# Optimization experiments

Hardware: AMD Instinct MI355X
Metric: run time of the kernel (lower is better)

## Reference

```python
import jax, jax.numpy as jnp
import numpy as np

N = 100000   # nodes
E = 800000   # undirected (unique) edges; directed count = 2*E
DV = 128; DE = 16; DH = 128; DO = 128
G = 64       # graphs in batch


def setup_inputs() -> dict:
    key = jax.random.key(0)
    ks = jax.random.split(key, 8)
    x = jax.random.normal(ks[0], (N, DV), jnp.float32)
    edge_index = jax.random.randint(ks[1], (2, 2 * E), 0, N, dtype=jnp.int32)
    edge_attr = jax.random.normal(ks[2], (E, DE), jnp.float32)
    batch = jnp.sort(jax.random.randint(ks[3], (N,), 0, G, dtype=jnp.int32))
    s = lambda k, shp, fan: jax.random.normal(k, shp, jnp.float32) / np.sqrt(fan)
    W_gcn = s(ks[4], (DV, DH), DV); b_gcn = jnp.zeros((DH,), jnp.float32)
    W_le = s(ks[5], (DE, DH), DE); b_le = jnp.zeros((DH,), jnp.float32)
    W_lin = s(ks[6], (2 * DH, DH), 2 * DH); b_lin = jnp.zeros((DH,), jnp.float32)
    W_out = s(ks[7], (DH, DO), DH); b_out = jnp.zeros((DO,), jnp.float32)
    return dict(x=x, edge_index=edge_index, edge_attr=edge_attr, batch=batch,
                W_gcn=W_gcn, b_gcn=b_gcn, W_le=W_le, b_le=b_le,
                W_lin=W_lin, b_lin=b_lin, W_out=W_out, b_out=b_out)


def reference(x, edge_index, edge_attr, batch,
              W_gcn, b_gcn, W_le, b_le, W_lin, b_lin, W_out, b_out):
    n = x.shape[0]
    loop = jnp.arange(n, dtype=edge_index.dtype)
    src = jnp.concatenate([edge_index[0], loop])  # [2E+N] with self loops
    dst = jnp.concatenate([edge_index[1], loop])

    # ---- GCNConv: symmetric norm, self-loops, lin then aggregate, + bias ----
    xw = x @ W_gcn                                      # [N, DH]
    ones_e = jnp.ones(src.shape[0], jnp.float32)
    deg = jax.ops.segment_sum(ones_e, dst, num_segments=n)  # >=1 via self loops
    dinv = jax.lax.rsqrt(deg)
    norm = dinv[src] * dinv[dst]                        # [2E+N]
    h = jax.ops.segment_sum(norm[:, None] * xw[src], dst, num_segments=n) + b_gcn
    h = jax.nn.relu(h)

    # ---- EdgeGCN: duplicate edge_attr per direction, self-loop attr = ones ----
    ea2 = jnp.repeat(edge_attr, 2, axis=0)              # [2E, DE] interleaved
    ea_full = jnp.concatenate([ea2, jnp.ones((n, edge_attr.shape[1]), jnp.float32)])
    edge_feat = ea_full @ W_le + b_le                   # [2E+N, DH]
    x_j = h[src]                                        # gather source node feats
    msg = jnp.concatenate([x_j, edge_feat], axis=-1) @ W_lin + b_lin
    h2 = jax.ops.segment_sum(msg, dst, num_segments=n)  # aggr='add'
    h2 = jax.nn.relu(h2)

    # ---- global mean pool + final linear ----
    cnt = jax.ops.segment_sum(jnp.ones(n, jnp.float32), batch, num_segments=G)
    pooled = jax.ops.segment_sum(h2, batch, num_segments=G) / jnp.maximum(cnt, 1.0)[:, None]
    return pooled @ W_out + b_out                       # [G, DO]
```

## Files before the change

### kernel.cpp

```cpp
#include <hip/hip_runtime.h>
#include <hip/hip_bf16.h>
#include <cstddef>

typedef unsigned int  u32;
typedef unsigned short u16;
typedef __attribute__((ext_vector_type(8))) short short8;
typedef __attribute__((ext_vector_type(4))) float f32x4;
typedef __attribute__((ext_vector_type(2))) float f32x2;

#define DV 128
#define DH 128
#define DE 16
#define DO 128

__device__ inline float bf_lo(u32 u){ return __uint_as_float(u << 16); }
__device__ inline float bf_hi(u32 u){ return __uint_as_float(u & 0xFFFF0000u); }
__device__ inline u32 fpack2(float a, float b){
  u32 ua = __float_as_uint(a), ub = __float_as_uint(b);
  ua += 0x7FFFu + ((ua >> 16) & 1u);
  ub += 0x7FFFu + ((ub >> 16) & 1u);
  return (ua >> 16) | (ub & 0xFFFF0000u);
}
__device__ inline u16 f2bf(float a){
  u32 ua = __float_as_uint(a); ua += 0x7FFFu + ((ua >> 16) & 1u); return (u16)(ua >> 16);
}

__device__ inline void acc_fp8v(u32 s, f32x2& lo, f32x2& hi){
  lo += __builtin_amdgcn_cvt_pk_f32_fp8((int)s, false);
  hi += __builtin_amdgcn_cvt_pk_f32_fp8((int)s, true);
}
__device__ inline u32 pack_fp8(float a0, float a1, float a2, float a3){
  int o = __builtin_amdgcn_cvt_pk_fp8_f32(a0, a1, 0, false);
  o = __builtin_amdgcn_cvt_pk_fp8_f32(a2, a3, o, true);
  return (u32)o;
}

__global__ void k_init(int* cnt, float* poolp, u32* xws_zrow, u32* h_zrow, int n, int pn){
  int v = blockIdx.x * blockDim.x + threadIdx.x;
  if (v < n) cnt[v] = 0;
  if (v < pn) poolp[v] = 0.f;
  if (v < 32){ xws_zrow[v] = 0u; h_zrow[v] = 0u; }
}

__global__ void k_count(const int* dst, const float* edge_attr, int* cnt, int* rank,
                        u32* ea_pack, int2* ce, int e2, int cefill, int nmark){
  int j = blockIdx.x * blockDim.x + threadIdx.x;
  int tot = gridDim.x * blockDim.x;
  if (j < e2){
    rank[j] = atomicAdd(&cnt[dst[j]], 1);
    float4 f0 = *(const float4*)(edge_attr + (size_t)j * 8);
    float4 f1 = *(const float4*)(edge_attr + (size_t)j * 8 + 4);
    uint4 o;
    o.x = fpack2(f0.x, f0.y); o.y = fpack2(f0.z, f0.w);
    o.z = fpack2(f1.x, f1.y); o.w = fpack2(f1.z, f1.w);
    *(uint4*)(ea_pack + (size_t)j * 4) = o;
  }
  int2 pd = make_int2(nmark, 0);
  for (int i = j; i < cefill; i += tot) ce[i] = pd;
}

__global__ __launch_bounds__(256) void k_scan1(const int* cnt, int* partial, int* bsums, int n){
  __shared__ int lds[256];
  int t = threadIdx.x;
  int base = blockIdx.x * 1024 + t * 4;
  int v0=0,v1=0,v2=0,v3=0;
  if (base + 3 < n){ int4 q = *(const int4*)(cnt + base); v0=q.x; v1=q.y; v2=q.z; v3=q.w; }
  else {
    if (base + 0 < n) v0 = cnt[base];
    if (base + 1 < n) v1 = cnt[base+1];
    if (base + 2 < n) v2 = cnt[base+2];
  }
  v0 = (v0 + 7) & ~7; v1 = (v1 + 7) & ~7; v2 = (v2 + 7) & ~7; v3 = (v3 + 7) & ~7;
  v1 += v0; v2 += v1; v3 += v2;
  lds[t] = v3; __syncthreads();
  for (int off = 1; off < 256; off <<= 1){
    int x = (t >= off) ? lds[t - off] : 0;
    __syncthreads();
    lds[t] += x;
    __syncthreads();
  }
  int add = (t > 0) ? lds[t - 1] : 0;
  if (base + 3 < n){
    int4 q; q.x = v0+add; q.y = v1+add; q.z = v2+add; q.w = v3+add;
    *(int4*)(partial + base) = q;
  } else {
    if (base + 0 < n) partial[base]   = v0 + add;
    if (base + 1 < n) partial[base+1] = v1 + add;
    if (base + 2 < n) partial[base+2] = v2 + add;
  }
  if (t == 255) bsums[blockIdx.x] = lds[255];
}

__global__ __launch_bounds__(256) void k_scan3w(const int* partial, const int* bsums, int nb,
                                                int* row_ptr, const int* cnt,
                                                float* dinv, float* degf,
                                                const int* batch, int* startg, int n, int g, int NB,
                                                const float* W_lin, const float* b_lin,
                                                const float* W_le, const float* b_le, float* Wfull){
  int bid = blockIdx.x;
  int t = threadIdx.x;
  if (bid >= NB){
    int r = (bid - NB) * 2 + (t >> 7), c = t & 127;
    if (r < DH){
      Wfull[r * DH + c] = W_lin[r * DH + c];
    } else if (r < DH + DE){
      int i = r - DH;
      float acc = 0.f;
      #pragma unroll 8
      for (int k = 0; k < DH; k += 4){
        float4 wl = *(const float4*)(W_le + i * DH + k);
        acc += wl.x * W_lin[(size_t)(DH + k    ) * DH + c];
        acc += wl.y * W_lin[(size_t)(DH + k + 1) * DH + c];
        acc += wl.z * W_lin[(size_t)(DH + k + 2) * DH + c];
        acc += wl.w * W_lin[(size_t)(DH + k + 3) * DH + c];
      }
      Wfull[r * DH + c] = acc;
    } else if (r == 144){
      float acc = b_lin[c];
      #pragma unroll 8
      for (int k = 0; k < DH; k += 4){
        float4 bl = *(const float4*)(b_le + k);
        acc += bl.x * W_lin[(size_t)(DH + k    ) * DH + c];
        acc += bl.y * W_lin[(size_t)(DH + k + 1) * DH + c];
        acc += bl.z * W_lin[(size_t)(DH + k + 2) * DH + c];
        acc += bl.w * W_lin[(size_t)(DH + k + 3) * DH + c];
      }
      Wfull[r * DH + c] = acc;
    } else if (r < 160){
      Wfull[r * DH + c] = 0.f;
    }
    return;
  }
  __shared__ int lds[128];
  if (t < 128) lds[t] = (t < nb) ? bsums[t] : 0;
  __syncthreads();
  for (int off = 1; off < 128; off <<= 1){
    int x = (t >= off && t < 128) ? lds[t - off] : 0;
    __syncthreads();
    if (t < 128) lds[t] += x;
    __syncthreads();
  }
  int i = bid * 256 + t;
  if (i < n){
    int chunk = i >> 10;
    int add = (chunk > 0) ? lds[chunk - 1] : 0;
    row_ptr[i + 1] = partial[i] + add;
    if (i == 0) row_ptr[0] = 0;
    float c = (float)(cnt[i] + 1);
    dinv[i] = rsqrtf(c);
    degf[i] = c;
    int b = batch[i];
    int prev = (i == 0) ? -1 : batch[i - 1];
    for (int q = prev + 1; q <= b; ++q) startg[q] = i;
    if (i == n - 1){ for (int q = b + 1; q <= g; ++q) startg[q] = n; }
  }
}

__global__ __launch_bounds__(256) void k_scatter_g1(const int* src, const int* dst, const int* rank,
                                                    const int* row_ptr, int2* ce, int e2, int SB,
                                                    const float* x, const float* W,
                                                    const float* dinv, u32* xws8, int M){
  __shared__ u16 lds_u[64 * 136];
  int bid = blockIdx.x;
  int tid = threadIdx.x;
  if (bid < SB){
    int j = bid * 256 + tid;
    if (j < e2){
      int d = dst[j];
      int pos = row_ptr[d] + rank[j];
      ce[pos] = make_int2(src[j] << 5, j >> 1);
    }
    return;
  }
  int row0 = (bid - SB) * 64;
  u16* Wt = lds_u;
  u16* At = lds_u + 128 * 40;
  int l = tid & 63, w = tid >> 6;
  int m = l & 15, quad = l >> 4;
  f32x4 acc[8];
  #pragma unroll
  for (int ct = 0; ct < 8; ++ct) acc[ct] = (f32x4){0.f, 0.f, 0.f, 0.f};
  for (int ks = 0; ks < DV; ks += 32){
    __syncthreads();
    {
      int c = tid & 127, hh = tid >> 7;
      #pragma unroll
      for (int g2 = 0; g2 < 2; ++g2){
        int k0 = hh * 16 + g2 * 8;
        const float* Wp = W + (size_t)(ks + k0) * 128 + c;
        float w0 = Wp[0*128], w1 = Wp[1*128], w2 = Wp[2*128], w3 = Wp[3*128];
        float w4 = Wp[4*128], w5 = Wp[5*128], w6 = Wp[6*128], w7 = Wp[7*128];
        uint4 pk;
        pk.x = fpack2(w0, w1); pk.y = fpack2(w2, w3);
        pk.z = fpack2(w4, w5); pk.w = fpack2(w6, w7);
        *(uint4*)&Wt[c * 40 + k0] = pk;
      }
    }
    {
      int r = tid >> 2, ch = tid & 3;
      int gr = row0 + r; if (gr > M - 1) gr = M - 1;
      const float* A = x + (size_t)gr * DV + ks + ch * 8;
      float4 q0 = *(const float4*)A;
      float4 q1 = *(const float4*)(A + 4);
      uint4 pk;
      pk.x = fpack2(q0.x, q0.y); pk.y = fpack2(q0.z, q0.w);
      pk.z = fpack2(q1.x, q1.y); pk.w = fpack2(q1.z, q1.w);
      *(uint4*)&At[r * 40 + ch * 8] = pk;
    }
    __syncthreads();
    short8 av = *(const short8*)&At[(w * 16 + m) * 40 + quad * 8];
    #pragma unroll
    for (int ct = 0; ct < 8; ++ct){
      short8 bv = *(const short8*)&Wt[(ct * 16 + m) * 40 + quad * 8];
      acc[ct] = __builtin_amdgcn_mfma_f32_16x16x32_bf16(av, bv, acc[ct], 0, 0, 0);
    }
  }
  __syncthreads();
  u16* Ct = lds_u;
  float sc[4];
  #pragma unroll
  for (int r = 0; r < 4; ++r){
    int gr = row0 + w * 16 + quad * 4 + r;
    sc[r] = dinv[gr < M ? gr : (M - 1)];
  }
  #pragma unroll
  for (int ct = 0; ct < 8; ++ct){
    #pragma unroll
    for (int r = 0; r < 4; ++r){
      float vv = acc[ct][r] * sc[r];
      Ct[(w * 16 + quad * 4 + r) * 136 + ct * 16 + m] = f2bf(vv);
    }
  }
  __syncthreads();
  for (int idx = tid; idx < 64 * 16; idx += 256){
    int r = idx >> 4, c8 = idx & 15;
    int gr = row0 + r;
    if (gr < M){
      uint4 qv = *(const uint4*)&Ct[r * 136 + c8 * 8];
      uint2 ov;
      ov.x = (u32)__builtin_amdgcn_cvt_pk_fp8_f32(bf_lo(qv.y), bf_hi(qv.y),
             __builtin_amdgcn_cvt_pk_fp8_f32(bf_lo(qv.x), bf_hi(qv.x), 0, false), true);
      ov.y = (u32)__builtin_amdgcn_cvt_pk_fp8_f32(bf_lo(qv.w), bf_hi(qv.w),
             __builtin_amdgcn_cvt_pk_fp8_f32(bf_lo(qv.z), bf_hi(qv.z), 0, false), true);
      *(uint2*)(xws8 + (size_t)gr * 32 + c8 * 2) = ov;
    }
  }
}

__global__ __launch_bounds__(256) void k_gemm2_pool(const u16* A2b, const float* W, int M,
                                                    const int* batchp, float* poolp){
  __shared__ u16 lds_u[128 * 40 + 64 * 40];
  u16* Wt = lds_u;
  u16* At = lds_u + 128 * 40;
  int tid = threadIdx.x;
  int row0 = blockIdx.x * 64;
  int l = tid & 63, w = tid >> 6;
  int m = l & 15, quad = l >> 4;
  f32x4 acc[8];
  #pragma unroll
  for (int ct = 0; ct < 8; ++ct) acc[ct] = (f32x4){0.f, 0.f, 0.f, 0.f};
  for (int ks = 0; ks < 160; ks += 32){
    __syncthreads();
    {
      int c = tid & 127, hh = tid >> 7;
      #pragma unroll
      for (int g2 = 0; g2 < 2; ++g2){
        int k0 = hh * 16 + g2 * 8;
        const float* Wp = W + (size_t)(ks + k0) * 128 + c;
        float w0 = Wp[0*128], w1 = Wp[1*128], w2 = Wp[2*128], w3 = Wp[3*128];
        float w4 = Wp[4*128], w5 = Wp[5*128], w6 = Wp[6*128], w7 = Wp[7*128];
        uint4 pk;
        pk.x = fpack2(w0, w1); pk.y = fpack2(w2, w3);
        pk.z = fpack2(w4, w5); pk.w = fpack2(w6, w7);
        *(uint4*)&Wt[c * 40 + k0] = pk;
      }
    }
    {
      int r = tid >> 2, ch = tid & 3;
      int gr = row0 + r; if (gr > M - 1) gr = M - 1;
      uint4 pk = *(const uint4*)(A2b + (size_t)gr * 160 + ks + ch * 8);
      *(uint4*)&At[r * 40 + ch * 8] = pk;
    }
    __syncthreads();
    short8 av = *(const short8*)&At[(w * 16 + m) * 40 + quad * 8];
    #pragma unroll
    for (int ct = 0; ct < 8; ++ct){
      short8 bv = *(const short8*)&Wt[(ct * 16 + m) * 40 + quad * 8];
      acc[ct] = __builtin_amdgcn_mfma_f32_16x16x32_bf16(av, bv, acc[ct], 0, 0, 0);
    }
  }
  __syncthreads();

  float* ps = (float*)lds_u;
  int rbase = w * 16 + quad * 4;
  int g0 = batchp[row0];
  int glast = batchp[(row0 + 63 < M) ? (row0 + 63) : (M - 1)];
  if (g0 == glast){
    #pragma unroll
    for (int ct = 0; ct < 8; ++ct){
      float s = 0.f;
      #pragma unroll
      for (int r = 0; r < 4; ++r){
        float vv = fmaxf(acc[ct][r], 0.f);
        if (row0 + rbase + r < M) s += vv;
      }
      s += __shfl_xor(s, 16);
      s += __shfl_xor(s, 32);
      if (quad == 0) ps[w * 128 + ct * 16 + m] = s;
    }
    __syncthreads();
    if (tid < 128){
      float t = ps[tid] + ps[128 + tid] + ps[256 + tid] + ps[384 + tid];
      atomicAdd(&poolp[g0 * DO + tid], t);
    }
  } else {
    #pragma unroll
    for (int ct = 0; ct < 8; ++ct){
      #pragma unroll
      for (int r = 0; r < 4; ++r){
        int row = row0 + rbase + r;
        if (row < M){
          float vv = fmaxf(acc[ct][r], 0.f);
          atomicAdd(&poolp[batchp[row] * DO + ct * 16 + m], vv);
        }
      }
    }
  }
}

__global__ __launch_bounds__(256) void k_phase1(const u32* xws8, const int* row_ptr, const int2* ce,
                                                const float* dinv, const float* b_gcn, u32* h8, int n){
  int lane = threadIdx.x & 63;
  int ln = lane & 31;
  int v = blockIdx.x * 8 + ((threadIdx.x >> 6) << 1) + (lane >> 5);
  if (v >= n) return;
  u32 sp = xws8[(size_t)v * 32 + ln];
  f32x2 aLo = (f32x2){0.f, 0.f}, aHi = (f32x2){0.f, 0.f};
  acc_fp8v(sp, aLo, aHi);
  int e0 = row_ptr[v], e1 = row_ptr[v + 1];
  int B = (e1 - e0) >> 3;
  const int4* cp = (const int4*)(ce + e0);
  u32 q0=0,q1=0,q2=0,q3=0,q4=0,q5=0,q6=0,q7=0;
  u32 r0=0,r1=0,r2=0,r3=0,r4=0,r5=0,r6=0,r7=0;
  if (B > 0){
    int4 A = cp[0], Bb = cp[1], C = cp[2], D = cp[3];
    q0 = xws8[A.x + ln]; q1 = xws8[A.z + ln];
    q2 = xws8[Bb.x + ln]; q3 = xws8[Bb.z + ln];
    q4 = xws8[C.x + ln]; q5 = xws8[C.z + ln];
    q6 = xws8[D.x + ln]; q7 = xws8[D.z + ln];
  }
  if (B > 1){
    int4 A = cp[4], Bb = cp[5], C = cp[6], D = cp[7];
    r0 = xws8[A.x + ln]; r1 = xws8[A.z + ln];
    r2 = xws8[Bb.x + ln]; r3 = xws8[Bb.z + ln];
    r4 = xws8[C.x + ln]; r5 = xws8[C.z + ln];
    r6 = xws8[D.x + ln]; r7 = xws8[D.z + ln];
  }
  for (int k = 0; k + 2 < B; ++k){
    const int4* cpp = cp + (size_t)(k + 2) * 4;
    int4 A = cpp[0], Bb = cpp[1], C = cpp[2], D = cpp[3];
    u32 p0 = xws8[A.x + ln], p1 = xws8[A.z + ln];
    u32 p2 = xws8[Bb.x + ln], p3 = xws8[Bb.z + ln];
    u32 p4 = xws8[C.x + ln], p5 = xws8[C.z + ln];
    u32 p6 = xws8[D.x + ln], p7 = xws8[D.z + ln];
    acc_fp8v(q0, aLo, aHi); acc_fp8v(q1, aLo, aHi);
    acc_fp8v(q2, aLo, aHi); acc_fp8v(q3, aLo, aHi);
    acc_fp8v(q4, aLo, aHi); acc_fp8v(q5, aLo, aHi);
    acc_fp8v(q6, aLo, aHi); acc_fp8v(q7, aLo, aHi);
    q0=r0; q1=r1; q2=r2; q3=r3; q4=r4; q5=r5; q6=r6; q7=r7;
    r0=p0; r1=p1; r2=p2; r3=p3; r4=p4; r5=p5; r6=p6; r7=p7;
  }
  if (B > 1){
    acc_fp8v(q0, aLo, aHi); acc_fp8v(q1, aLo, aHi);
    acc_fp8v(q2, aLo, aHi); acc_fp8v(q3, aLo, aHi);
    acc_fp8v(q4, aLo, aHi); acc_fp8v(q5, aLo, aHi);
    acc_fp8v(q6, aLo, aHi); acc_fp8v(q7, aLo, aHi);
    q0=r0; q1=r1; q2=r2; q3=r3; q4=r4; q5=r5; q6=r6; q7=r7;
  }
  if (B > 0){
    acc_fp8v(q0, aLo, aHi); acc_fp8v(q1, aLo, aHi);
    acc_fp8v(q2, aLo, aHi); acc_fp8v(q3, aLo, aHi);
    acc_fp8v(q4, aLo, aHi); acc_fp8v(q5, aLo, aHi);
    acc_fp8v(q6, aLo, aHi); acc_fp8v(q7, aLo, aHi);
  }
  float dv = dinv[v];
  float4 bg = *(const float4*)(b_gcn + ln * 4);
  float a0 = fmaxf(fmaf(dv, aLo.x, bg.x), 0.f);
  float a1 = fmaxf(fmaf(dv, aLo.y, bg.y), 0.f);
  float a2 = fmaxf(fmaf(dv, aHi.x, bg.z), 0.f);
  float a3 = fmaxf(fmaf(dv, aHi.y, bg.w), 0.f);
  h8[(size_t)v * 32 + ln] = pack_fp8(a0, a1, a2, a3);
}

__global__ __launch_bounds__(256) void k_phase2(const u32* h8, const int* row_ptr, const int2* ce,
                                                const u16* ea_bf, const float* degf,
                                                u16* A2b, int n){
  int lane = threadIdx.x & 63;
  int ln = lane & 31;
  int half = lane >> 5;
  int v = blockIdx.x * 8 + ((threadIdx.x >> 6) << 1) + half;
  if (v >= n) return;
  u32 sp = h8[(size_t)v * 32 + ln];
  f32x2 aLo = (f32x2){0.f, 0.f}, aHi = (f32x2){0.f, 0.f};
  acc_fp8v(sp, aLo, aHi);
  float es = 0.f;
  int ch = ln & 15, grp = ln >> 4;
  int nmark = n << 5;
  int e0 = row_ptr[v], e1 = row_ptr[v + 1];
  int i = e0;
  u32 q0=0,q1=0,q2=0,q3=0,q4=0,q5=0,q6=0,q7=0;
  float w0=0.f,w1=0.f,w2=0.f,w3=0.f;
  float m0=0.f,m1=0.f,m2=0.f,m3=0.f;
  if (i < e1){
    const int4* cp = (const int4*)(ce + i);
    int4 A = cp[0], B = cp[1], C = cp[2], D = cp[3];
    q0 = h8[A.x + ln]; q1 = h8[A.z + ln];
    q2 = h8[B.x + ln]; q3 = h8[B.z + ln];
    q4 = h8[C.x + ln]; q5 = h8[C.z + ln];
    q6 = h8[D.x + ln]; q7 = h8[D.z + ln];
    int s0x = grp ? C.x : A.x, s0e = grp ? C.y : A.y;
    int s1x = grp ? C.z : A.z, s1e = grp ? C.w : A.w;
    int s2x = grp ? D.x : B.x, s2e = grp ? D.y : B.y;
    int s3x = grp ? D.z : B.z, s3e = grp ? D.w : B.w;
    w0 = bf_lo((u32)ea_bf[(size_t)s0e * 16 + ch]);
    w1 = bf_lo((u32)ea_bf[(size_t)s1e * 16 + ch]);
    w2 = bf_lo((u32)ea_bf[(size_t)s2e * 16 + ch]);
    w3 = bf_lo((u32)ea_bf[(size_t)s3e * 16 + ch]);
    m0 = (s0x != nmark) ? 1.f : 0.f;
    m1 = (s1x != nmark) ? 1.f : 0.f;
    m2 = (s2x != nmark) ? 1.f : 0.f;
    m3 = (s3x != nmark) ? 1.f : 0.f;
  }
  for (; i + 8 < e1; i += 8){
    const int4* cp2 = (const int4*)(ce + i + 8);
    int4 A2 = cp2[0], B2 = cp2[1], C2 = cp2[2], D2 = cp2[3];
    int t0x = grp ? C2.x : A2.x, t0e = grp ? C2.y : A2.y;
    int t1x = grp ? C2.z : A2.z, t1e = grp ? C2.w : A2.w;
    int t2x = grp ? D2.x : B2.x, t2e = grp ? D2.y : B2.y;
    int t3x = grp ? D2.z : B2.z, t3e = grp ? D2.w : B2.w;
    float u0 = bf_lo((u32)ea_bf[(size_t)t0e * 16 + ch]);
    float u1 = bf_lo((u32)ea_bf[(size_t)t1e * 16 + ch]);
    float u2 = bf_lo((u32)ea_bf[(size_t)t2e * 16 + ch]);
    float u3 = bf_lo((u32)ea_bf[(size_t)t3e * 16 + ch]);
    float n0 = (t0x != nmark) ? 1.f : 0.f;
    float n1 = (t1x != nmark) ? 1.f : 0.f;
    float n2 = (t2x != nmark) ? 1.f : 0.f;
    float n3 = (t3x != nmark) ? 1.f : 0.f;
    u32 p0 = h8[A2.x + ln], p1 = h8[A2.z + ln];
    u32 p2 = h8[B2.x + ln], p3 = h8[B2.z + ln];
    u32 p4 = h8[C2.x + ln], p5 = h8[C2.z + ln];
    u32 p6 = h8[D2.x + ln], p7 = h8[D2.z + ln];
    acc_fp8v(q0, aLo, aHi); acc_fp8v(q1, aLo, aHi);
    acc_fp8v(q2, aLo, aHi); acc_fp8v(q3, aLo, aHi);
    acc_fp8v(q4, aLo, aHi); acc_fp8v(q5, aLo, aHi);
    acc_fp8v(q6, aLo, aHi); acc_fp8v(q7, aLo, aHi);
    es = fmaf(m0, w0, es);
    es = fmaf(m1, w1, es);
    es = fmaf(m2, w2, es);
    es = fmaf(m3, w3, es);
    q0=p0; q1=p1; q2=p2; q3=p3; q4=p4; q5=p5; q6=p6; q7=p7;
    w0=u0; w1=u1; w2=u2; w3=u3;
    m0=n0; m1=n1; m2=n2; m3=n3;
  }
  if (i < e1){
    acc_fp8v(q0, aLo, aHi); acc_fp8v(q1, aLo, aHi);
    acc_fp8v(q2, aLo, aHi); acc_fp8v(q3, aLo, aHi);
    acc_fp8v(q4, aLo, aHi); acc_fp8v(q5, aLo, aHi);
    acc_fp8v(q6, aLo, aHi); acc_fp8v(q7, aLo, aHi);
    es = fmaf(m0, w0, es);
    es = fmaf(m1, w1, es);
    es = fmaf(m2, w2, es);
    es = fmaf(m3, w3, es);
  }
  es += __shfl_xor(es, 16);
  float c0v = __shfl(es, half * 32 + (ln & 7) * 2);
  float c1v = __shfl(es, half * 32 + (ln & 7) * 2 + 1);
  u32* rowp = (u32*)(A2b + (size_t)v * 160);
  uint2 o; o.x = fpack2(aLo.x, aLo.y); o.y = fpack2(aHi.x, aHi.y);
  *(uint2*)(rowp + ln * 2) = o;
  if (ln < 8){
    rowp[64 + ln] = fpack2(c0v + 1.0f, c1v + 1.0f);
  } else if (ln < 16){
    rowp[64 + ln] = (ln == 8) ? (u32)f2bf(degf[v]) : 0u;
  }
}

__global__ __launch_bounds__(128) void k_poolb_final(const float* poolp, const int* start,
                                                     const float* W_out, const float* b_out,
                                                     float* out){
  __shared__ float pl[DH];
  int g = blockIdx.x, c = threadIdx.x;
  int cntg = start[g + 1] - start[g]; if (cntg < 1) cntg = 1;
  pl[c] = poolp[g * DO + c] / (float)cntg;
  __syncthreads();
  float acc = b_out[c];
  for (int k = 0; k < DH; ++k) acc += pl[k] * W_out[k * DO + c];
  out[g * DO + c] = acc;
}

extern "C" void kernel_launch(void* const* d_in, const int* in_sizes, int n_in,
                              void* d_out, int out_size, void* d_ws, size_t ws_size,
                              hipStream_t stream){
  const float* x         = (const float*)d_in[0];
  const int*   edge_index= (const int*)  d_in[1];
  const float* edge_attr = (const float*)d_in[2];
  const int*   batch     = (const int*)  d_in[3];
  const float* W_gcn     = (const float*)d_in[4];
  const float* b_gcn     = (const float*)d_in[5];
  const float* W_le      = (const float*)d_in[6];
  const float* b_le      = (const float*)d_in[7];
  const float* W_lin     = (const float*)d_in[8];
  const float* b_lin     = (const float*)d_in[9];
  const float* W_out     = (const float*)d_in[10];
  const float* b_out     = (const float*)d_in[11];
  float* out = (float*)d_out;

  const int n  = in_sizes[0] / DV;
  const int e2 = in_sizes[1] / 2;
  const int g  = out_size / DO;
  const int* srcp = edge_index;
  const int* dstp = edge_index + e2;
  const int e2pad = e2 + 7 * n + 8;

  char* ws = (char*)d_ws;
  size_t off = 0;
  auto alloc = [&](size_t bytes) -> char* {
    char* p = ws + off; off = (off + bytes + 255) & ~(size_t)255; return p;
  };

  int*   cnt     = (int*)  alloc((size_t)n * 4);
  int*   row_ptr = (int*)  alloc((size_t)(n + 1) * 4);
  int*   rank    = (int*)  alloc((size_t)e2 * 4);
  int*   partial = (int*)  alloc((size_t)n * 4);
  int*   bsums   = (int*)  alloc(512);
  float* dinv    = (float*)alloc((size_t)n * 4);
  float* degf    = (float*)alloc((size_t)n * 4);
  int*   startg  = (int*)  alloc((size_t)(g + 1) * 4);
  float* poolp   = (float*)alloc((size_t)g * DO * 4);
  float* Wfull   = (float*)alloc(160 * DH * 4);
  u32*   h8      = (u32*)  alloc((size_t)(n + 1) * 128);
  int2*  ce      = (int2*) alloc((size_t)e2pad * 8);
  u32*   ea_bf   = (u32*)  alloc((size_t)e2 * 16);
  size_t szXW = (size_t)(n + 1) * 128, szA2 = (size_t)n * 160 * 2;
  char* regionA = alloc(szA2 > szXW ? szA2 : szXW);
  u32* xws8 = (u32*)regionA;
  u16* A2b  = (u16*)regionA;

  const int nb1024 = (n + 1023) / 1024;
  const int NB = (n + 255) / 256;
  const int SB = (e2 + 255) / 256;
  const int GB = (n + 63) / 64;

  k_init      <<<(n + 255) / 256, 256, 0, stream>>>(cnt, poolp,
                                                    xws8 + (size_t)n * 32, h8 + (size_t)n * 32,
                                                    n, g * DO);
  k_count     <<<SB, 256, 0, stream>>>(dstp, edge_attr, cnt, rank, ea_bf, ce,
                                       e2, e2pad, n << 5);
  k_scan1     <<<nb1024, 256, 0, stream>>>(cnt, partial, bsums, n);
  k_scan3w    <<<NB + 80, 256, 0, stream>>>(partial, bsums, nb1024, row_ptr, cnt, dinv, degf,
                                            batch, startg, n, g, NB,
                                            W_lin, b_lin, W_le, b_le, Wfull);
  k_scatter_g1<<<SB + GB, 256, 0, stream>>>(srcp, dstp, rank, row_ptr, ce, e2, SB,
                                            x, W_gcn, dinv, xws8, n);
  k_phase1    <<<(n + 7) / 8, 256, 0, stream>>>(xws8, row_ptr, ce, dinv, b_gcn, h8, n);
  k_phase2    <<<(n + 7) / 8, 256, 0, stream>>>(h8, row_ptr, ce,
                                                (const u16*)ea_bf, degf, A2b, n);
  k_gemm2_pool<<<GB, 256, 0, stream>>>(A2b, Wfull, n, batch, poolp);
  k_poolb_final<<<g, 128, 0, stream>>>(poolp, startg, W_out, b_out, out);
}
```

Before: 398.8 us.

## Fuse phase-2 edge aggregation with final GEMM and pooling via LDS staging

```diff
diff --git a/kernel.cpp b/kernel.cpp
--- a/kernel.cpp
+++ b/kernel.cpp
@@ -247,87 +247,6 @@
   }
 }
 
-__global__ __launch_bounds__(256) void k_gemm2_pool(const u16* A2b, const float* W, int M,
-                                                    const int* batchp, float* poolp){
-  __shared__ u16 lds_u[128 * 40 + 64 * 40];
-  u16* Wt = lds_u;
-  u16* At = lds_u + 128 * 40;
-  int tid = threadIdx.x;
-  int row0 = blockIdx.x * 64;
-  int l = tid & 63, w = tid >> 6;
-  int m = l & 15, quad = l >> 4;
-  f32x4 acc[8];
-  #pragma unroll
-  for (int ct = 0; ct < 8; ++ct) acc[ct] = (f32x4){0.f, 0.f, 0.f, 0.f};
-  for (int ks = 0; ks < 160; ks += 32){
-    __syncthreads();
-    {
-      int c = tid & 127, hh = tid >> 7;
-      #pragma unroll
-      for (int g2 = 0; g2 < 2; ++g2){
-        int k0 = hh * 16 + g2 * 8;
-        const float* Wp = W + (size_t)(ks + k0) * 128 + c;
-        float w0 = Wp[0*128], w1 = Wp[1*128], w2 = Wp[2*128], w3 = Wp[3*128];
-        float w4 = Wp[4*128], w5 = Wp[5*128], w6 = Wp[6*128], w7 = Wp[7*128];
-        uint4 pk;
-        pk.x = fpack2(w0, w1); pk.y = fpack2(w2, w3);
-        pk.z = fpack2(w4, w5); pk.w = fpack2(w6, w7);
-        *(uint4*)&Wt[c * 40 + k0] = pk;
-      }
-    }
-    {
-      int r = tid >> 2, ch = tid & 3;
-      int gr = row0 + r; if (gr > M - 1) gr = M - 1;
-      uint4 pk = *(const uint4*)(A2b + (size_t)gr * 160 + ks + ch * 8);
-      *(uint4*)&At[r * 40 + ch * 8] = pk;
-    }
-    __syncthreads();
-    short8 av = *(const short8*)&At[(w * 16 + m) * 40 + quad * 8];
-    #pragma unroll
-    for (int ct = 0; ct < 8; ++ct){
-      short8 bv = *(const short8*)&Wt[(ct * 16 + m) * 40 + quad * 8];
-      acc[ct] = __builtin_amdgcn_mfma_f32_16x16x32_bf16(av, bv, acc[ct], 0, 0, 0);
-    }
-  }
-  __syncthreads();
-
-  float* ps = (float*)lds_u;
-  int rbase = w * 16 + quad * 4;
-  int g0 = batchp[row0];
-  int glast = batchp[(row0 + 63 < M) ? (row0 + 63) : (M - 1)];
-  if (g0 == glast){
-    #pragma unroll
-    for (int ct = 0; ct < 8; ++ct){
-      float s = 0.f;
-      #pragma unroll
-      for (int r = 0; r < 4; ++r){
-        float vv = fmaxf(acc[ct][r], 0.f);
-        if (row0 + rbase + r < M) s += vv;
-      }
-      s += __shfl_xor(s, 16);
-      s += __shfl_xor(s, 32);
-      if (quad == 0) ps[w * 128 + ct * 16 + m] = s;
-    }
-    __syncthreads();
-    if (tid < 128){
-      float t = ps[tid] + ps[128 + tid] + ps[256 + tid] + ps[384 + tid];
-      atomicAdd(&poolp[g0 * DO + tid], t);
-    }
-  } else {
-    #pragma unroll
-    for (int ct = 0; ct < 8; ++ct){
-      #pragma unroll
-      for (int r = 0; r < 4; ++r){
-        int row = row0 + rbase + r;
-        if (row < M){
-          float vv = fmaxf(acc[ct][r], 0.f);
-          atomicAdd(&poolp[batchp[row] * DO + ct * 16 + m], vv);
-        }
-      }
-    }
-  }
-}
-
 __global__ __launch_bounds__(256) void k_phase1(const u32* xws8, const int* row_ptr, const int2* ce,
                                                 const float* dinv, const float* b_gcn, u32* h8, int n){
   int lane = threadIdx.x & 63;
@@ -392,96 +311,177 @@
   h8[(size_t)v * 32 + ln] = pack_fp8(a0, a1, a2, a3);
 }
 
-__global__ __launch_bounds__(256) void k_phase2(const u32* h8, const int* row_ptr, const int2* ce,
+__global__ __launch_bounds__(256) void k_p2gemm(const u32* h8, const int* row_ptr, const int2* ce,
                                                 const u16* ea_bf, const float* degf,
-                                                u16* A2b, int n){
-  int lane = threadIdx.x & 63;
+                                                const float* W, int n,
+                                                const int* batchp, float* poolp){
+  __shared__ u16 At2[64 * 172];
+  __shared__ u16 Wt[128 * 40];
+  int tid = threadIdx.x;
+  int lane = tid & 63;
   int ln = lane & 31;
   int half = lane >> 5;
-  int v = blockIdx.x * 8 + ((threadIdx.x >> 6) << 1) + half;
-  if (v >= n) return;
-  u32 sp = h8[(size_t)v * 32 + ln];
-  f32x2 aLo = (f32x2){0.f, 0.f}, aHi = (f32x2){0.f, 0.f};
-  acc_fp8v(sp, aLo, aHi);
-  float es = 0.f;
+  int row0 = blockIdx.x * 64;
   int ch = ln & 15, grp = ln >> 4;
   int nmark = n << 5;
-  int e0 = row_ptr[v], e1 = row_ptr[v + 1];
-  int i = e0;
-  u32 q0=0,q1=0,q2=0,q3=0,q4=0,q5=0,q6=0,q7=0;
-  float w0=0.f,w1=0.f,w2=0.f,w3=0.f;
-  float m0=0.f,m1=0.f,m2=0.f,m3=0.f;
-  if (i < e1){
-    const int4* cp = (const int4*)(ce + i);
-    int4 A = cp[0], B = cp[1], C = cp[2], D = cp[3];
-    q0 = h8[A.x + ln]; q1 = h8[A.z + ln];
-    q2 = h8[B.x + ln]; q3 = h8[B.z + ln];
-    q4 = h8[C.x + ln]; q5 = h8[C.z + ln];
-    q6 = h8[D.x + ln]; q7 = h8[D.z + ln];
-    int s0x = grp ? C.x : A.x, s0e = grp ? C.y : A.y;
-    int s1x = grp ? C.z : A.z, s1e = grp ? C.w : A.w;
-    int s2x = grp ? D.x : B.x, s2e = grp ? D.y : B.y;
-    int s3x = grp ? D.z : B.z, s3e = grp ? D.w : B.w;
-    w0 = bf_lo((u32)ea_bf[(size_t)s0e * 16 + ch]);
-    w1 = bf_lo((u32)ea_bf[(size_t)s1e * 16 + ch]);
-    w2 = bf_lo((u32)ea_bf[(size_t)s2e * 16 + ch]);
-    w3 = bf_lo((u32)ea_bf[(size_t)s3e * 16 + ch]);
-    m0 = (s0x != nmark) ? 1.f : 0.f;
-    m1 = (s1x != nmark) ? 1.f : 0.f;
-    m2 = (s2x != nmark) ? 1.f : 0.f;
-    m3 = (s3x != nmark) ? 1.f : 0.f;
-  }
-  for (; i + 8 < e1; i += 8){
-    const int4* cp2 = (const int4*)(ce + i + 8);
-    int4 A2 = cp2[0], B2 = cp2[1], C2 = cp2[2], D2 = cp2[3];
-    int t0x = grp ? C2.x : A2.x, t0e = grp ? C2.y : A2.y;
-    int t1x = grp ? C2.z : A2.z, t1e = grp ? C2.w : A2.w;
-    int t2x = grp ? D2.x : B2.x, t2e = grp ? D2.y : B2.y;
-    int t3x = grp ? D2.z : B2.z, t3e = grp ? D2.w : B2.w;
-    float u0 = bf_lo((u32)ea_bf[(size_t)t0e * 16 + ch]);
-    float u1 = bf_lo((u32)ea_bf[(size_t)t1e * 16 + ch]);
-    float u2 = bf_lo((u32)ea_bf[(size_t)t2e * 16 + ch]);
-    float u3 = bf_lo((u32)ea_bf[(size_t)t3e * 16 + ch]);
-    float n0 = (t0x != nmark) ? 1.f : 0.f;
-    float n1 = (t1x != nmark) ? 1.f : 0.f;
-    float n2 = (t2x != nmark) ? 1.f : 0.f;
-    float n3 = (t3x != nmark) ? 1.f : 0.f;
-    u32 p0 = h8[A2.x + ln], p1 = h8[A2.z + ln];
-    u32 p2 = h8[B2.x + ln], p3 = h8[B2.z + ln];
-    u32 p4 = h8[C2.x + ln], p5 = h8[C2.z + ln];
-    u32 p6 = h8[D2.x + ln], p7 = h8[D2.z + ln];
-    acc_fp8v(q0, aLo, aHi); acc_fp8v(q1, aLo, aHi);
-    acc_fp8v(q2, aLo, aHi); acc_fp8v(q3, aLo, aHi);
-    acc_fp8v(q4, aLo, aHi); acc_fp8v(q5, aLo, aHi);
-    acc_fp8v(q6, aLo, aHi); acc_fp8v(q7, aLo, aHi);
-    es = fmaf(m0, w0, es);
-    es = fmaf(m1, w1, es);
-    es = fmaf(m2, w2, es);
-    es = fmaf(m3, w3, es);
-    q0=p0; q1=p1; q2=p2; q3=p3; q4=p4; q5=p5; q6=p6; q7=p7;
-    w0=u0; w1=u1; w2=u2; w3=u3;
-    m0=n0; m1=n1; m2=n2; m3=n3;
-  }
-  if (i < e1){
-    acc_fp8v(q0, aLo, aHi); acc_fp8v(q1, aLo, aHi);
-    acc_fp8v(q2, aLo, aHi); acc_fp8v(q3, aLo, aHi);
-    acc_fp8v(q4, aLo, aHi); acc_fp8v(q5, aLo, aHi);
-    acc_fp8v(q6, aLo, aHi); acc_fp8v(q7, aLo, aHi);
-    es = fmaf(m0, w0, es);
-    es = fmaf(m1, w1, es);
-    es = fmaf(m2, w2, es);
-    es = fmaf(m3, w3, es);
-  }
-  es += __shfl_xor(es, 16);
-  float c0v = __shfl(es, half * 32 + (ln & 7) * 2);
-  float c1v = __shfl(es, half * 32 + (ln & 7) * 2 + 1);
-  u32* rowp = (u32*)(A2b + (size_t)v * 160);
-  uint2 o; o.x = fpack2(aLo.x, aLo.y); o.y = fpack2(aHi.x, aHi.y);
-  *(uint2*)(rowp + ln * 2) = o;
-  if (ln < 8){
-    rowp[64 + ln] = fpack2(c0v + 1.0f, c1v + 1.0f);
-  } else if (ln < 16){
-    rowp[64 + ln] = (ln == 8) ? (u32)f2bf(degf[v]) : 0u;
+
+  for (int pass = 0; pass < 8; ++pass){
+    int local = pass * 8 + ((tid >> 6) << 1) + half;
+    int v = row0 + local;
+    u32* rowp = (u32*)&At2[(size_t)local * 172];
+    if (v >= n){
+      rowp[ln] = 0u; rowp[ln + 32] = 0u;
+      if (ln < 22) rowp[ln + 64] = 0u;
+      continue;
+    }
+    u32 sp = h8[(size_t)v * 32 + ln];
+    f32x2 aLo = (f32x2){0.f, 0.f}, aHi = (f32x2){0.f, 0.f};
+    acc_fp8v(sp, aLo, aHi);
+    float es = 0.f;
+    int e0 = row_ptr[v], e1 = row_ptr[v + 1];
+    int i = e0;
+    u32 q0=0,q1=0,q2=0,q3=0,q4=0,q5=0,q6=0,q7=0;
+    float w0=0.f,w1=0.f,w2=0.f,w3=0.f;
+    float m0=0.f,m1=0.f,m2=0.f,m3=0.f;
+    if (i < e1){
+      const int4* cp = (const int4*)(ce + i);
+      int4 A = cp[0], B = cp[1], C = cp[2], D = cp[3];
+      q0 = h8[A.x + ln]; q1 = h8[A.z + ln];
+      q2 = h8[B.x + ln]; q3 = h8[B.z + ln];
+      q4 = h8[C.x + ln]; q5 = h8[C.z + ln];
+      q6 = h8[D.x + ln]; q7 = h8[D.z + ln];
+      int s0x = grp ? C.x : A.x, s0e = grp ? C.y : A.y;
+      int s1x = grp ? C.z : A.z, s1e = grp ? C.w : A.w;
+      int s2x = grp ? D.x : B.x, s2e = grp ? D.y : B.y;
+      int s3x = grp ? D.z : B.z, s3e = grp ? D.w : B.w;
+      w0 = bf_lo((u32)ea_bf[(size_t)s0e * 16 + ch]);
+      w1 = bf_lo((u32)ea_bf[(size_t)s1e * 16 + ch]);
+      w2 = bf_lo((u32)ea_bf[(size_t)s2e * 16 + ch]);
+      w3 = bf_lo((u32)ea_bf[(size_t)s3e * 16 + ch]);
+      m0 = (s0x != nmark) ? 1.f : 0.f;
+      m1 = (s1x != nmark) ? 1.f : 0.f;
+      m2 = (s2x != nmark) ? 1.f : 0.f;
+      m3 = (s3x != nmark) ? 1.f : 0.f;
+    }
+    for (; i + 8 < e1; i += 8){
+      const int4* cp2 = (const int4*)(ce + i + 8);
+      int4 A2 = cp2[0], B2 = cp2[1], C2 = cp2[2], D2 = cp2[3];
+      int t0x = grp ? C2.x : A2.x, t0e = grp ? C2.y : A2.y;
+      int t1x = grp ? C2.z : A2.z, t1e = grp ? C2.w : A2.w;
+      int t2x = grp ? D2.x : B2.x, t2e = grp ? D2.y : B2.y;
+      int t3x = grp ? D2.z : B2.z, t3e = grp ? D2.w : B2.w;
+      float u0 = bf_lo((u32)ea_bf[(size_t)t0e * 16 + ch]);
+      float u1 = bf_lo((u32)ea_bf[(size_t)t1e * 16 + ch]);
+      float u2 = bf_lo((u32)ea_bf[(size_t)t2e * 16 + ch]);
+      float u3 = bf_lo((u32)ea_bf[(size_t)t3e * 16 + ch]);
+      float n0 = (t0x != nmark) ? 1.f : 0.f;
+      float n1 = (t1x != nmark) ? 1.f : 0.f;
+      float n2 = (t2x != nmark) ? 1.f : 0.f;
+      float n3 = (t3x != nmark) ? 1.f : 0.f;
+      u32 p0 = h8[A2.x + ln], p1 = h8[A2.z + ln];
+      u32 p2 = h8[B2.x + ln], p3 = h8[B2.z + ln];
+      u32 p4 = h8[C2.x + ln], p5 = h8[C2.z + ln];
+      u32 p6 = h8[D2.x + ln], p7 = h8[D2.z + ln];
+      acc_fp8v(q0, aLo, aHi); acc_fp8v(q1, aLo, aHi);
+      acc_fp8v(q2, aLo, aHi); acc_fp8v(q3, aLo, aHi);
+      acc_fp8v(q4, aLo, aHi); acc_fp8v(q5, aLo, aHi);
+      acc_fp8v(q6, aLo, aHi); acc_fp8v(q7, aLo, aHi);
+      es = fmaf(m0, w0, es);
+      es = fmaf(m1, w1, es);
+      es = fmaf(m2, w2, es);
+      es = fmaf(m3, w3, es);
+      q0=p0; q1=p1; q2=p2; q3=p3; q4=p4; q5=p5; q6=p6; q7=p7;
+      w0=u0; w1=u1; w2=u2; w3=u3;
+      m0=n0; m1=n1; m2=n2; m3=n3;
+    }
+    if (i < e1){
+      acc_fp8v(q0, aLo, aHi); acc_fp8v(q1, aLo, aHi);
+      acc_fp8v(q2, aLo, aHi); acc_fp8v(q3, aLo, aHi);
+      acc_fp8v(q4, aLo, aHi); acc_fp8v(q5, aLo, aHi);
+      acc_fp8v(q6, aLo, aHi); acc_fp8v(q7, aLo, aHi);
+      es = fmaf(m0, w0, es);
+      es = fmaf(m1, w1, es);
+      es = fmaf(m2, w2, es);
+      es = fmaf(m3, w3, es);
+    }
+    es += __shfl_xor(es, 16);
+    float c0v = __shfl(es, half * 32 + (ln & 7) * 2);
+    float c1v = __shfl(es, half * 32 + (ln & 7) * 2 + 1);
+    uint2 o; o.x = fpack2(aLo.x, aLo.y); o.y = fpack2(aHi.x, aHi.y);
+    *(uint2*)(rowp + ln * 2) = o;
+    if (ln < 8){
+      rowp[64 + ln] = fpack2(c0v + 1.0f, c1v + 1.0f);
+    } else if (ln < 16){
+      rowp[64 + ln] = (ln == 8) ? (u32)f2bf(degf[v]) : 0u;
+    }
+  }
+  __syncthreads();
+
+  int l = tid & 63, w = tid >> 6;
+  int m = l & 15, quad = l >> 4;
+  f32x4 acc[8];
+  #pragma unroll
+  for (int ct = 0; ct < 8; ++ct) acc[ct] = (f32x4){0.f, 0.f, 0.f, 0.f};
+  for (int ks = 0; ks < 160; ks += 32){
+    __syncthreads();
+    {
+      int c = tid & 127, hh = tid >> 7;
+      #pragma unroll
+      for (int g2 = 0; g2 < 2; ++g2){
+        int k0 = hh * 16 + g2 * 8;
+        const float* Wp = W + (size_t)(ks + k0) * 128 + c;
+        float w0 = Wp[0*128], w1 = Wp[1*128], w2 = Wp[2*128], w3 = Wp[3*128];
+        float w4 = Wp[4*128], w5 = Wp[5*128], w6 = Wp[6*128], w7 = Wp[7*128];
+        uint4 pk;
+        pk.x = fpack2(w0, w1); pk.y = fpack2(w2, w3);
+        pk.z = fpack2(w4, w5); pk.w = fpack2(w6, w7);
+        *(uint4*)&Wt[c * 40 + k0] = pk;
+      }
+    }
+    __syncthreads();
+    short8 av = *(const short8*)&At2[(w * 16 + m) * 172 + ks + quad * 8];
+    #pragma unroll
+    for (int ct = 0; ct < 8; ++ct){
+      short8 bv = *(const short8*)&Wt[(ct * 16 + m) * 40 + quad * 8];
+      acc[ct] = __builtin_amdgcn_mfma_f32_16x16x32_bf16(av, bv, acc[ct], 0, 0, 0);
+    }
+  }
+  __syncthreads();
+
+  float* ps = (float*)Wt;
+  int rbase = w * 16 + quad * 4;
+  int g0 = batchp[row0];
+  int glast = batchp[(row0 + 63 < n) ? (row0 + 63) : (n - 1)];
+  if (g0 == glast){
+    #pragma unroll
+    for (int ct = 0; ct < 8; ++ct){
+      float s = 0.f;
+      #pragma unroll
+      for (int r = 0; r < 4; ++r){
+        float vv = fmaxf(acc[ct][r], 0.f);
+        if (row0 + rbase + r < n) s += vv;
+      }
+      s += __shfl_xor(s, 16);
+      s += __shfl_xor(s, 32);
+      if (quad == 0) ps[w * 128 + ct * 16 + m] = s;
+    }
+    __syncthreads();
+    if (tid < 128){
+      float t = ps[tid] + ps[128 + tid] + ps[256 + tid] + ps[384 + tid];
+      atomicAdd(&poolp[g0 * DO + tid], t);
+    }
+  } else {
+    #pragma unroll
+    for (int ct = 0; ct < 8; ++ct){
+      #pragma unroll
+      for (int r = 0; r < 4; ++r){
+        int row = row0 + rbase + r;
+        if (row < n){
+          float vv = fmaxf(acc[ct][r], 0.f);
+          atomicAdd(&poolp[batchp[row] * DO + ct * 16 + m], vv);
+        }
+      }
+    }
   }
 }
 
@@ -541,10 +541,7 @@
   u32*   h8      = (u32*)  alloc((size_t)(n + 1) * 128);
   int2*  ce      = (int2*) alloc((size_t)e2pad * 8);
   u32*   ea_bf   = (u32*)  alloc((size_t)e2 * 16);
-  size_t szXW = (size_t)(n + 1) * 128, szA2 = (size_t)n * 160 * 2;
-  char* regionA = alloc(szA2 > szXW ? szA2 : szXW);
-  u32* xws8 = (u32*)regionA;
-  u16* A2b  = (u16*)regionA;
+  u32*   xws8    = (u32*)  alloc((size_t)(n + 1) * 128);
 
   const int nb1024 = (n + 1023) / 1024;
   const int NB = (n + 255) / 256;
@@ -563,8 +560,7 @@
   k_scatter_g1<<<SB + GB, 256, 0, stream>>>(srcp, dstp, rank, row_ptr, ce, e2, SB,
                                             x, W_gcn, dinv, xws8, n);
   k_phase1    <<<(n + 7) / 8, 256, 0, stream>>>(xws8, row_ptr, ce, dinv, b_gcn, h8, n);
-  k_phase2    <<<(n + 7) / 8, 256, 0, stream>>>(h8, row_ptr, ce,
-                                                (const u16*)ea_bf, degf, A2b, n);
-  k_gemm2_pool<<<GB, 256, 0, stream>>>(A2b, Wfull, n, batch, poolp);
+  k_p2gemm    <<<GB, 256, 0, stream>>>(h8, row_ptr, ce, (const u16*)ea_bf, degf,
+                                       Wfull, n, batch, poolp);
   k_poolb_final<<<g, 128, 0, stream>>>(poolp, startg, W_out, b_out, out);
 }
```

Result: no change. 392.0 us (-1.7%).
